# Kernel tuning notes

Measured on AMD Instinct MI355X. Metric: run time of the kernel, lower is better.

The kernel has to match this reference:

```python
import jax, jax.numpy as jnp
import numpy as np
import math

T, C, S = 16, 4, 256
DT = 0.05
JITTER = 1e-05
IDENTITY_MIX = 0.05
MIN_BLOCK_SCALE = 0.01
CLIP = 1e4
MAX_TRIES = 8


def _sym(m):
    return 0.5 * (m + jnp.swapaxes(m, -1, -2))


def _san_m(m):
    return _sym(jnp.clip(jnp.nan_to_num(m, nan=0.0, posinf=CLIP, neginf=-CLIP), -CLIP, CLIP))


def _san_v(v):
    return jnp.clip(jnp.nan_to_num(v, nan=0.0, posinf=CLIP, neginf=-CLIP), -CLIP, CLIP)


def _stable_inv_logdet(mat, base_jitter):
    # mat: [..., 2, 2] symmetric. Vectorized closed-form version of the per-block
    # Cholesky retry loop: for a 2x2 SPD matrix [[a,b],[b,c]], cholesky succeeds
    # iff a > 0 and det = a*c - b^2 > 0; inverse = adj/det; logdet = log(det).
    eye = jnp.eye(2, dtype=mat.dtype)
    cand = _san_m(mat)
    diag = jnp.diagonal(cand, axis1=-2, axis2=-1)                    # [..., 2]
    diag_scale = jnp.maximum(jnp.mean(jnp.abs(diag), axis=-1), 1.0)  # [...]
    j0 = max(base_jitter, 1e-6)
    jitters = j0 * (10.0 ** jnp.arange(MAX_TRIES, dtype=mat.dtype))  # [K]
    jit_b = jitters.reshape((MAX_TRIES,) + (1,) * diag_scale.ndim) * diag_scale[None]  # [K, ...]
    rep = _san_m(cand[None] + jit_b[..., None, None] * eye)          # [K, ..., 2, 2]
    a, b, c = rep[..., 0, 0], rep[..., 0, 1], rep[..., 1, 1]
    det = a * c - b * b
    ok = (a > 0) & (det > 0)
    idx = jnp.argmax(ok, axis=0)                                     # first successful jitter level
    any_ok = jnp.any(ok, axis=0)
    gather = lambda x: jnp.take_along_axis(x, idx[None], axis=0)[0]
    a0, b0, c0 = gather(a), gather(b), gather(c)
    det0 = jnp.where(any_ok, a0 * c0 - b0 * b0, 1.0)
    rep0 = jnp.take_along_axis(rep, idx[None, ..., None, None], axis=0)[0]
    inv0 = jnp.stack([jnp.stack([c0, -b0], -1), jnp.stack([-b0, a0], -1)], -2) / det0[..., None, None]
    inv0 = _san_m(inv0)
    logdet0 = jnp.nan_to_num(jnp.log(det0), nan=0.0, posinf=20.0, neginf=-20.0)
    # fallback: all tries failed -> diagonal repair
    jit_f = j0 * (10.0 ** MAX_TRIES)
    sd = jnp.nan_to_num(diag, nan=1.0, posinf=CLIP, neginf=1.0)
    sd = jnp.maximum(jnp.abs(sd), (jit_f * diag_scale)[..., None] + 1e-4)
    rep_f = _san_m(sd[..., None] * eye + (jit_f * diag_scale)[..., None, None] * eye)
    dg_f = jnp.maximum(jnp.diagonal(rep_f, axis1=-2, axis2=-1), 1e-6)
    inv_f = _san_m((1.0 / dg_f)[..., None] * eye)
    logdet_f = jnp.nan_to_num(jnp.sum(jnp.log(dg_f), -1), nan=0.0, posinf=20.0, neginf=-20.0)
    m = any_ok[..., None, None]
    repaired = jnp.where(m, rep0, rep_f)
    inverse = jnp.where(m, inv0, inv_f)
    log_det = jnp.where(any_ok, logdet0, logdet_f)
    return repaired, inverse, log_det


def setup_inputs() -> dict:
    key = jax.random.key(0)
    k1, k2, k3 = jax.random.split(key, 3)
    means = jax.random.normal(k1, (T, C, 2), dtype=jnp.float32)
    covariances = jax.random.normal(k2, (T, C, 2, 2), dtype=jnp.float32)
    site_coords = jax.random.normal(k3, (S, 2), dtype=jnp.float32) * 3.0
    block_scale_raw = jnp.full((C, C), 0.25, dtype=jnp.float32).at[jnp.arange(C), jnp.arange(C)].set(1.0)
    identity_mix_logit = jnp.asarray(math.log(IDENTITY_MIX / (1.0 - IDENTITY_MIX)), dtype=jnp.float32)
    return {"means": means, "covariances": covariances, "site_coords": site_coords,
            "block_scale_raw": block_scale_raw, "identity_mix_logit": identity_mix_logit}


def reference(means, covariances, site_coords, block_scale_raw, identity_mix_logit):
    means = _san_v(means)                                              # [T, C, 2]
    covs = _san_m(covariances)                                         # [T, C, 2, 2]
    lags = _san_v(site_coords[:, None, :] - site_coords[None, :, :])   # [S, S, 2]
    scales = jax.nn.softplus(block_scale_raw) + MIN_BLOCK_SCALE        # [C, C]
    mix = jax.nn.sigmoid(identity_mix_logit)
    eye2 = jnp.eye(2, dtype=means.dtype)
    drift = _san_v(DT * (means[:, :, None, :] - means[:, None, :, :])) # [T, C, C, 2]
    disp = eye2 + 2.0 * DT ** 2 * (covs[:, :, None] + covs[:, None, :])
    disp = _san_m(disp + JITTER * eye2)
    disp, inv, logdet = _stable_inv_logdet(disp, JITTER)               # [T,C,C,2,2], [T,C,C]
    centered = _san_v(lags[None, None, None] - drift[:, :, :, None, None, :])  # [T,C,C,S,S,2]
    quad = jnp.einsum('tijabk,tijkl,tijabl->tijab', centered, inv, centered)
    quad = jnp.clip(jnp.nan_to_num(quad, nan=0.0, posinf=60.0, neginf=0.0), 0.0, 60.0)
    expo = jnp.clip(-0.5 * logdet[..., None, None] - quad, -60.0, 20.0)
    block = jnp.nan_to_num(scales[None, :, :, None, None] * jnp.exp(expo), nan=0.0, posinf=0.0, neginf=0.0)
    t, c, s = means.shape[0], means.shape[1], site_coords.shape[0]
    # blocks laid out row-major in (component, site): index (i*S+a, j*S+b)
    K = jnp.transpose(block, (0, 1, 3, 2, 4)).reshape(t, c * s, c * s)
    tr = jnp.nan_to_num(K / jnp.maximum(K.sum(-1, keepdims=True), JITTER), nan=0.0, posinf=0.0, neginf=0.0)
    tr = tr / jnp.maximum(tr.sum(-1, keepdims=True), JITTER)
    ident = jnp.eye(c * s, dtype=tr.dtype)
    tr = (1.0 - mix) * tr + mix * ident
    tr = jnp.nan_to_num(tr, nan=0.0, posinf=0.0, neginf=0.0)
    tr = tr / jnp.maximum(tr.sum(-1, keepdims=True), JITTER)
    return tr, drift, disp, scales, mix
```

## Files before the change

### kernel.cpp

```cpp
#include <hip/hip_runtime.h>
#include <math.h>

#define T_ 16
#define C_ 4
#define S_ 256
static constexpr float DT      = 0.05f;
static constexpr float JITTER  = 1e-5f;
static constexpr float CLIPV   = 1e4f;

static constexpr int TR_SIZE     = T_ * (C_ * S_) * (C_ * S_);
static constexpr int DRIFT_OFF   = TR_SIZE;
static constexpr int DISP_OFF    = DRIFT_OFF + T_ * C_ * C_ * 2;
static constexpr int SCALES_OFF  = DISP_OFF + T_ * C_ * C_ * 4;
static constexpr int MIX_OFF     = SCALES_OFF + C_ * C_;

static constexpr int WS_REC = 8;
static constexpr int WS_MIX = T_ * C_ * C_ * WS_REC;

__device__ __forceinline__ float sanv(float x) {
    if (isnan(x)) return 0.f;
    return fminf(fmaxf(x, -CLIPV), CLIPV);
}

__global__ __launch_bounds__(256)
void prep_kernel(const float* __restrict__ means,
                 const float* __restrict__ covs,
                 const float* __restrict__ bsr,
                 const float* __restrict__ mixlogit,
                 float* __restrict__ out,
                 float* __restrict__ ws) {
    int tid = threadIdx.x;
    if (tid >= T_ * C_ * C_) return;
    int t = tid >> 4;
    int i = (tid >> 2) & 3;
    int j = tid & 3;
    int bl = tid;

    float mix_ = sanv(means[(t * C_ + i) * 2 + 0]);
    float miy  = sanv(means[(t * C_ + i) * 2 + 1]);
    float mjx  = sanv(means[(t * C_ + j) * 2 + 0]);
    float mjy  = sanv(means[(t * C_ + j) * 2 + 1]);
    float dx = sanv(DT * (mix_ - mjx));
    float dy = sanv(DT * (miy - mjy));
    out[DRIFT_OFF + bl * 2 + 0] = dx;
    out[DRIFT_OFF + bl * 2 + 1] = dy;

    const float* ci = covs + (t * C_ + i) * 4;
    const float* cj = covs + (t * C_ + j) * 4;
    float ci00 = sanv(ci[0]), ci01 = 0.5f * (sanv(ci[1]) + sanv(ci[2])), ci11 = sanv(ci[3]);
    float cj00 = sanv(cj[0]), cj01 = 0.5f * (sanv(cj[1]) + sanv(cj[2])), cj11 = sanv(cj[3]);

    const float k2 = 2.0f * DT * DT;
    float a = sanv(1.0f + k2 * (ci00 + cj00) + JITTER);
    float b = sanv(        k2 * (ci01 + cj01));
    float c = sanv(1.0f + k2 * (ci11 + cj11) + JITTER);

    float ds = fmaxf(0.5f * (fabsf(a) + fabsf(c)), 1.0f);
    float ra = 0.f, rb = 0.f, rc = 0.f, det0 = 1.f;
    bool found = false;
    float jit = 1e-5f;
    #pragma unroll
    for (int k = 0; k < 8; ++k) {
        float ja = sanv(a + jit * ds);
        float jb = sanv(b);
        float jc = sanv(c + jit * ds);
        float det = ja * jc - jb * jb;
        if (!found && ja > 0.f && det > 0.f) {
            found = true; ra = ja; rb = jb; rc = jc; det0 = det;
        }
        jit *= 10.f;
    }

    float i00, i01, i11, ld, o00, o01, o11;
    if (found) {
        i00 = sanv(rc / det0);
        i01 = sanv(-rb / det0);
        i11 = sanv(ra / det0);
        ld = logf(det0);
        if (isnan(ld)) ld = 0.f;
        else if (isinf(ld)) ld = (ld > 0.f) ? 20.f : -20.f;
        o00 = ra; o01 = rb; o11 = rc;
    } else {
        float jf = 1e3f;
        float sd0 = fmaxf(fabsf(a), jf * ds + 1e-4f);
        float sd1 = fmaxf(fabsf(c), jf * ds + 1e-4f);
        o00 = sanv(sd0 + jf * ds); o11 = sanv(sd1 + jf * ds); o01 = 0.f;
        float dg0 = fmaxf(o00, 1e-6f), dg1 = fmaxf(o11, 1e-6f);
        i00 = sanv(1.f / dg0); i11 = sanv(1.f / dg1); i01 = 0.f;
        ld = logf(dg0) + logf(dg1);
        if (isnan(ld)) ld = 0.f;
        else if (isinf(ld)) ld = (ld > 0.f) ? 20.f : -20.f;
    }
    out[DISP_OFF + bl * 4 + 0] = o00;
    out[DISP_OFF + bl * 4 + 1] = o01;
    out[DISP_OFF + bl * 4 + 2] = o01;
    out[DISP_OFF + bl * 4 + 3] = o11;

    float x = bsr[i * 4 + j];
    float sc = fmaxf(x, 0.f) + log1pf(expf(-fabsf(x))) + 0.01f;
    if (t == 0) out[SCALES_OFF + i * 4 + j] = sc;

    float* w = ws + bl * WS_REC;
    w[0] = i00; w[1] = i01; w[2] = i11; w[3] = ld;
    w[4] = dx;  w[5] = dy;  w[6] = sc;  w[7] = 0.f;

    if (tid == 0) {
        float lg = mixlogit[0];
        float mx = 1.f / (1.f + expf(-lg));
        out[MIX_OFF] = mx;
        ws[WS_MIX]   = mx;
    }
}

__device__ __forceinline__ float block_reduce_sum(float v, float* sdata) {
    #pragma unroll
    for (int off = 32; off > 0; off >>= 1) v += __shfl_down(v, off, 64);
    int lane = threadIdx.x & 63, w = threadIdx.x >> 6;
    if (lane == 0) sdata[w] = v;
    __syncthreads();
    return sdata[0] + sdata[1] + sdata[2] + sdata[3];
}

__global__ __launch_bounds__(256)
void row_kernel(const float* __restrict__ site,
                const float* __restrict__ ws,
                float* __restrict__ tr) {
    __shared__ float sdata[4];
    int r = blockIdx.x;
    int t = r >> 10;
    int i = (r >> 8) & 3;
    int a = r & 255;
    int tid = threadIdx.x;

    float2 sb = ((const float2*)site)[tid];
    float2 sa = ((const float2*)site)[a];
    float lx = sa.x - sb.x, ly = sa.y - sb.y;
    float mx = ws[WS_MIX];

    float v[4];
    #pragma unroll
    for (int m = 0; m < 4; ++m) {
        const float* w = ws + ((t * C_ + i) * C_ + m) * WS_REC;
        float i00 = w[0], i01 = w[1], i11 = w[2], ld = w[3];
        float dx = w[4], dy = w[5], sc = w[6];
        float cx = lx - dx, cy = ly - dy;
        float q = i00 * cx * cx + 2.f * i01 * cx * cy + i11 * cy * cy;
        q = fminf(fmaxf(q, 0.f), 60.f);
        float e = fminf(fmaxf(-0.5f * ld - q, -60.f), 20.f);
        v[m] = sc * __expf(e);
    }

    float s1 = block_reduce_sum(v[0] + v[1] + v[2] + v[3], sdata);
    float d1 = fmaxf(s1, JITTER);
    float s2 = s1 / d1;
    float d2 = fmaxf(s2, JITTER);
    float sum_t2 = s2 / d2;
    float s3 = (1.f - mx) * sum_t2 + mx;
    float d3 = fmaxf(s3, JITTER);
    float scale = (1.f - mx) / (d1 * d2 * d3);
    float diag  = mx / d3;

    size_t base = ((size_t)t << 20) + (size_t)(i * S_ + a) * 1024;
    #pragma unroll
    for (int m = 0; m < 4; ++m) {
        float o = v[m] * scale;
        if (m == i && tid == a) o += diag;
        tr[base + m * S_ + tid] = o;
    }
}

extern "C" void kernel_launch(void* const* d_in, const int* in_sizes, int n_in,
                              void* d_out, int out_size, void* d_ws, size_t ws_size,
                              hipStream_t stream) {
    const float* means    = (const float*)d_in[0];
    const float* covs     = (const float*)d_in[1];
    const float* site     = (const float*)d_in[2];
    const float* bsr      = (const float*)d_in[3];
    const float* mixlogit = (const float*)d_in[4];
    float* out = (float*)d_out;
    float* ws  = (float*)d_ws;

    prep_kernel<<<1, 256, 0, stream>>>(means, covs, bsr, mixlogit, out, ws);
    row_kernel<<<T_ * C_ * S_, 256, 0, stream>>>(site, ws, out);
}
```

Baseline: 95.39 us.

## Remap row kernel to per-wave components with vectorized nontemporal stores

Each wave of the row kernel now handles one destination component and each lane computes four consecutive sites, so every thread issues one 16-byte nontemporal store instead of four scalar stores. Per-component parameters become wave-uniform, the -0.5*logdet scaling is precomputed in the prep kernel, and the divisions are replaced with hardware reciprocal approximations. This targets store throughput and instruction count on a write-bound 64 MB output, at the cost of slightly different rounding from the approximate reciprocals.

```diff
diff --git a/kernel.cpp b/kernel.cpp
--- a/kernel.cpp
+++ b/kernel.cpp
@@ -7,6 +7,8 @@
 static constexpr float DT      = 0.05f;
 static constexpr float JITTER  = 1e-5f;
 static constexpr float CLIPV   = 1e4f;
+
+typedef float f32x4 __attribute__((ext_vector_type(4)));
 
 static constexpr int TR_SIZE     = T_ * (C_ * S_) * (C_ * S_);
 static constexpr int DRIFT_OFF   = TR_SIZE;
@@ -101,7 +103,7 @@
     if (t == 0) out[SCALES_OFF + i * 4 + j] = sc;
 
     float* w = ws + bl * WS_REC;
-    w[0] = i00; w[1] = i01; w[2] = i11; w[3] = ld;
+    w[0] = i00; w[1] = i01; w[2] = i11; w[3] = -0.5f * ld;
     w[4] = dx;  w[5] = dy;  w[6] = sc;  w[7] = 0.f;
 
     if (tid == 0) {
@@ -110,15 +112,6 @@
         out[MIX_OFF] = mx;
         ws[WS_MIX]   = mx;
     }
-}
-
-__device__ __forceinline__ float block_reduce_sum(float v, float* sdata) {
-    #pragma unroll
-    for (int off = 32; off > 0; off >>= 1) v += __shfl_down(v, off, 64);
-    int lane = threadIdx.x & 63, w = threadIdx.x >> 6;
-    if (lane == 0) sdata[w] = v;
-    __syncthreads();
-    return sdata[0] + sdata[1] + sdata[2] + sdata[3];
 }
 
 __global__ __launch_bounds__(256)
@@ -131,42 +124,68 @@
     int i = (r >> 8) & 3;
     int a = r & 255;
     int tid = threadIdx.x;
-
-    float2 sb = ((const float2*)site)[tid];
+    int lane = tid & 63;
+    int wid = __builtin_amdgcn_readfirstlane(tid >> 6);
+
+    const f32x4* s4 = (const f32x4*)site;
+    f32x4 p0 = s4[2 * lane];
+    f32x4 p1 = s4[2 * lane + 1];
     float2 sa = ((const float2*)site)[a];
-    float lx = sa.x - sb.x, ly = sa.y - sb.y;
     float mx = ws[WS_MIX];
+
+    const float* w = ws + ((t * C_ + i) * C_ + wid) * WS_REC;
+    float i00 = w[0], i01 = w[1], i11 = w[2], h = w[3];
+    float dx = w[4],  dy = w[5],  sc = w[6];
+    float ox = sa.x - dx, oy = sa.y - dy;
+
+    float bx[4] = {p0.x, p0.z, p1.x, p1.z};
+    float by[4] = {p0.y, p0.w, p1.y, p1.w};
 
     float v[4];
     #pragma unroll
-    for (int m = 0; m < 4; ++m) {
-        const float* w = ws + ((t * C_ + i) * C_ + m) * WS_REC;
-        float i00 = w[0], i01 = w[1], i11 = w[2], ld = w[3];
-        float dx = w[4], dy = w[5], sc = w[6];
-        float cx = lx - dx, cy = ly - dy;
-        float q = i00 * cx * cx + 2.f * i01 * cx * cy + i11 * cy * cy;
+    for (int k = 0; k < 4; ++k) {
+        float cx = ox - bx[k], cy = oy - by[k];
+        float u = i00 * cx + i01 * cy;
+        float z = i01 * cx + i11 * cy;
+        float q = cx * u + cy * z;
         q = fminf(fmaxf(q, 0.f), 60.f);
-        float e = fminf(fmaxf(-0.5f * ld - q, -60.f), 20.f);
-        v[m] = sc * __expf(e);
-    }
-
-    float s1 = block_reduce_sum(v[0] + v[1] + v[2] + v[3], sdata);
+        float e = fminf(fmaxf(h - q, -60.f), 20.f);
+        v[k] = sc * __expf(e);
+    }
+
+    float local = (v[0] + v[1]) + (v[2] + v[3]);
+    #pragma unroll
+    for (int off = 32; off > 0; off >>= 1) local += __shfl_down(local, off, 64);
+    if (lane == 0) sdata[wid] = local;
+    __syncthreads();
+    float s1 = sdata[0] + sdata[1] + sdata[2] + sdata[3];
+
     float d1 = fmaxf(s1, JITTER);
-    float s2 = s1 / d1;
+    float r1 = __builtin_amdgcn_rcpf(d1);
+    float s2 = s1 * r1;
     float d2 = fmaxf(s2, JITTER);
-    float sum_t2 = s2 / d2;
-    float s3 = (1.f - mx) * sum_t2 + mx;
+    float r2 = __builtin_amdgcn_rcpf(d2);
+    float sum_t2 = s2 * r2;
+    float omx = 1.f - mx;
+    float s3 = omx * sum_t2 + mx;
     float d3 = fmaxf(s3, JITTER);
-    float scale = (1.f - mx) / (d1 * d2 * d3);
-    float diag  = mx / d3;
+    float r3 = __builtin_amdgcn_rcpf(d3);
+    float scale = omx * r1 * r2 * r3;
+    float diag  = mx * r3;
+
+    f32x4 o;
+    o.x = v[0] * scale; o.y = v[1] * scale;
+    o.z = v[2] * scale; o.w = v[3] * scale;
+    if (wid == i && lane == (a >> 2)) {
+        int sl = a & 3;
+        if      (sl == 0) o.x += diag;
+        else if (sl == 1) o.y += diag;
+        else if (sl == 2) o.z += diag;
+        else              o.w += diag;
+    }
 
     size_t base = ((size_t)t << 20) + (size_t)(i * S_ + a) * 1024;
-    #pragma unroll
-    for (int m = 0; m < 4; ++m) {
-        float o = v[m] * scale;
-        if (m == i && tid == a) o += diag;
-        tr[base + m * S_ + tid] = o;
-    }
+    __builtin_nontemporal_store(o, (f32x4*)(tr + base) + tid);
 }
 
 extern "C" void kernel_launch(void* const* d_in, const int* in_sizes, int n_in,
```

Result: no change. 93.83 us (-1.6%).
